# Kernel tuning notes

Hardware: AMD Instinct MI355X
Metric: run time of the kernel (lower is better)

## Reference

```python
import jax, jax.numpy as jnp
import numpy as np


def setup_inputs() -> dict:
    key = jax.random.key(0)
    kq, kk, kv = jax.random.split(key, 3)
    B, H, S, D = 2, 8, 4096, 64
    return {
        "query": jax.random.normal(kq, (B, H, S, D), dtype=jnp.float32),
        "key": jax.random.normal(kk, (B, H, S, D), dtype=jnp.float32),
        "value": jax.random.normal(kv, (B, H, S, D), dtype=jnp.float32),
    }


def reference(query, key, value):
    # NOTE: the torch source overwrites sqrt(d) with d, so the divisor is D, not sqrt(D).
    d = query.shape[-1]
    # score: [B, H, S_q, S_k]
    score = jnp.einsum("bhqd,bhkd->bhqk", query, key) / d
    relu = jax.nn.relu(score)  # no softmax / row normalization
    out = jnp.einsum("bhqk,bhkd->bhqd", relu, value)
    return out
```

## Files before the change

kernel.cpp:

```cpp
#include <hip/hip_runtime.h>
#include <hip/hip_bf16.h>
#include <stdint.h>


#define NH 16
#define SEQ 4096
#define DD 64
#define HE (SEQ*DD)
#define HB (HE*2)
#define Q16_OFF 0
#define K16_OFF (NH*HB)
#define V16_OFF (2*NH*HB)
#define WS_NEED (3*NH*HB)

typedef __attribute__((ext_vector_type(8)))  short    bf16x8;
typedef __attribute__((ext_vector_type(16))) float    f32x16;
typedef __attribute__((ext_vector_type(4)))  uint32_t u32x4;

__device__ inline uint32_t f2bf1(float f) {
  return (uint32_t)__builtin_bit_cast(unsigned short, __float2bfloat16(f));
}
__device__ inline uint32_t pack2bf(float a, float b) {
  return f2bf1(a) | (f2bf1(b) << 16);
}
__device__ inline uint32_t cvtpk(float lo, float hi) {
  uint32_t r;
  asm("v_cvt_pk_bf16_f32 %0, %1, %2" : "=v"(r) : "v"(lo), "v"(hi));
  return r;
}
__device__ inline uint32_t relu2(uint32_t w) {
  uint32_t r;
  asm("v_pk_max_f16 %0, %1, 0" : "=v"(r) : "v"(w));
  return r;
}

__global__ __launch_bounds__(256) void prepass_kernel(const float* __restrict__ Q,
                                                      const float* __restrict__ K,
                                                      const float* __restrict__ V,
                                                      char* __restrict__ ws) {
  __shared__ float vt[64*65];
  int bx = blockIdx.x, tid = threadIdx.x;
  if (bx < 2048) {
    int head = bx >> 7, qg = bx & 127;
    int r31 = tid & 31, c = tid >> 5;
    const float4* s = (const float4*)(Q + (size_t)head*HE + ((size_t)(qg*32 + r31))*64 + c*8);
    float4 a = s[0], b = s[1];
    const float sc = 1.0f/64.0f;
    u32x4 o;
    o.x = pack2bf(a.x*sc, a.y*sc);
    o.y = pack2bf(a.z*sc, a.w*sc);
    o.z = pack2bf(b.x*sc, b.y*sc);
    o.w = pack2bf(b.z*sc, b.w*sc);
    char* tb = ws + Q16_OFF + (size_t)head*HB;
    *(u32x4*)(tb + ((qg*4 + (c >> 1))*1024) + ((c & 1)*32 + r31)*16) = o;
  } else if (bx < 3072) {
    int tile = bx - 2048;
    int head = tile >> 6, t = tile & 63;
    int r = tid >> 2, c0 = (tid & 3) * 16;
    const float4* s4 = (const float4*)(K + (size_t)head*HE + ((size_t)(t*64 + r))*64 + c0);
    float4 f0 = s4[0], f1 = s4[1], f2 = s4[2], f3 = s4[3];
    u32x4 c_lo, c_hi;
    c_lo.x = pack2bf(f0.x, f0.y); c_lo.y = pack2bf(f0.z, f0.w);
    c_lo.z = pack2bf(f1.x, f1.y); c_lo.w = pack2bf(f1.z, f1.w);
    c_hi.x = pack2bf(f2.x, f2.y); c_hi.y = pack2bf(f2.z, f2.w);
    c_hi.z = pack2bf(f3.x, f3.y); c_hi.w = pack2bf(f3.z, f3.w);
    char* tb = ws + K16_OFF + ((size_t)head*64 + t)*8192;
    char* chunk = tb + ((r >> 5)*4 + (tid & 3))*1024 + (r & 31)*16;
    *(u32x4*)(chunk)       = c_lo;
    *(u32x4*)(chunk + 512) = c_hi;
  } else {
    int tile = bx - 3072;
    int head = tile >> 6, t = tile & 63;
    int k = tid >> 2, c0 = (tid & 3)*16;
    const float4* s4 = (const float4*)(V + (size_t)head*HE + ((size_t)(t*64 + k))*64 + c0);
    float4 f0 = s4[0], f1 = s4[1], f2 = s4[2], f3 = s4[3];
    float tmp[16] = {f0.x,f0.y,f0.z,f0.w, f1.x,f1.y,f1.z,f1.w,
                     f2.x,f2.y,f2.z,f2.w, f3.x,f3.y,f3.z,f3.w};
    #pragma unroll
    for (int j = 0; j < 16; ++j) vt[k*65 + c0 + j] = tmp[j];
    __syncthreads();
    int d = tid >> 2, k0 = (tid & 3)*16;
    float v2[16];
    #pragma unroll
    for (int j = 0; j < 16; ++j) v2[j] = vt[(k0 + j)*65 + d];
    u32x4 c_lo, c_hi;
    c_lo.x = pack2bf(v2[0],  v2[1]);  c_lo.y = pack2bf(v2[2],  v2[3]);
    c_lo.z = pack2bf(v2[4],  v2[5]);  c_lo.w = pack2bf(v2[6],  v2[7]);
    c_hi.x = pack2bf(v2[8],  v2[9]);  c_hi.y = pack2bf(v2[10], v2[11]);
    c_hi.z = pack2bf(v2[12], v2[13]); c_hi.w = pack2bf(v2[14], v2[15]);
    char* tb = ws + V16_OFF + ((size_t)head*64 + t)*8192;
    char* chunk = tb + ((d >> 5)*4 + (tid & 3))*1024 + (d & 31)*16;
    *(u32x4*)(chunk)       = c_lo;
    *(u32x4*)(chunk + 512) = c_hi;
  }
}

__global__ __launch_bounds__(256, 2) void attn_kernel(const char* __restrict__ ws,
                                                      float* __restrict__ out) {
  __shared__ float red[128*64];
  int bid = blockIdx.x;
  int bx = (bid & 7) * 64 + (bid >> 3);
  int head = bx >> 5, qblk = bx & 31;
  int tid = threadIdx.x;
  int lane = tid & 63, w = tid >> 6;
  int l31 = lane & 31, h = lane >> 5;
  int g  = w >> 1;
  int wg = w & 1;

  const char* q16   = ws + Q16_OFF + (size_t)head*HB;
  const char* kbase = ws + K16_OFF + (size_t)head*HB + (size_t)g*32*8192;
  const char* vbase = ws + V16_OFF + (size_t)head*HB + (size_t)g*32*8192;

  int qg0 = qblk*4 + wg*2;
  bf16x8 qf[2][4];
  #pragma unroll
  for (int m = 0; m < 2; ++m)
    #pragma unroll
    for (int t = 0; t < 4; ++t)
      qf[m][t] = *(const bf16x8*)(q16 + ((size_t)((qg0 + m)*4 + t))*1024 + lane*16);

  f32x16 kZero;
  #pragma unroll
  for (int i = 0; i < 16; ++i) kZero[i] = 0.f;

  f32x16 o[2][2];
  #pragma unroll
  for (int m = 0; m < 2; ++m)
    #pragma unroll
    for (int nd = 0; nd < 2; ++nd)
      #pragma unroll
      for (int i = 0; i < 16; ++i) o[m][nd][i] = 0.f;

  bf16x8 kfA[2][4], kfB[2][4], vf[2][4];

  auto loadK = [&](bf16x8 (&kf)[2][4], int kt) {
    const char* kp = kbase + (size_t)kt*8192;
    #pragma unroll
    for (int i = 0; i < 8; ++i)
      kf[i >> 2][i & 3] = *(const bf16x8*)(kp + i*1024 + lane*16);
  };
  auto loadV = [&](int kt) {
    const char* vp = vbase + (size_t)kt*8192;
    #pragma unroll
    for (int i = 0; i < 8; ++i)
      vf[i >> 2][i & 3] = *(const bf16x8*)(vp + i*1024 + lane*16);
  };

  auto computeT = [&](bf16x8 (&kf)[2][4]) {
    f32x16 st[2][2];
    #pragma unroll
    for (int n = 0; n < 2; ++n) {
      __builtin_amdgcn_s_setprio(1);
      #pragma unroll
      for (int m = 0; m < 2; ++m) {
        f32x16 acc = __builtin_amdgcn_mfma_f32_32x32x16_bf16(kf[n][0], qf[m][0], kZero, 0, 0, 0);
        #pragma unroll
        for (int t = 1; t < 4; ++t)
          acc = __builtin_amdgcn_mfma_f32_32x32x16_bf16(kf[n][t], qf[m][t], acc, 0, 0, 0);
        st[m][n] = acc;
      }
      __builtin_amdgcn_s_setprio(0);
    }
    bf16x8 pa[2][4];
    #pragma unroll
    for (int m = 0; m < 2; ++m)
      #pragma unroll
      for (int n = 0; n < 2; ++n)
        #pragma unroll
        for (int kn = 0; kn < 2; ++kn) {
          uint32_t w0 = cvtpk(st[m][n][kn*8+0], st[m][n][kn*8+1]);
          uint32_t w1 = cvtpk(st[m][n][kn*8+2], st[m][n][kn*8+3]);
          uint32_t w2 = cvtpk(st[m][n][kn*8+4], st[m][n][kn*8+5]);
          uint32_t w3 = cvtpk(st[m][n][kn*8+6], st[m][n][kn*8+7]);
          asm("v_permlane32_swap_b32 %0, %1" : "+v"(w0), "+v"(w2));
          asm("v_permlane32_swap_b32 %0, %1" : "+v"(w1), "+v"(w3));
          union { uint32_t u[4]; bf16x8 v; } pk;
          pk.u[0] = relu2(w0);
          pk.u[1] = relu2(w1);
          pk.u[2] = relu2(w2);
          pk.u[3] = relu2(w3);
          pa[m][n*2 + kn] = pk.v;
        }
    __builtin_amdgcn_s_setprio(1);
    #pragma unroll
    for (int m = 0; m < 2; ++m)
      #pragma unroll
      for (int nd = 0; nd < 2; ++nd)
        #pragma unroll
        for (int ks = 0; ks < 4; ++ks)
          o[m][nd] = __builtin_amdgcn_mfma_f32_32x32x16_bf16(pa[m][ks], vf[nd][ks], o[m][nd], 0, 0, 0);
    __builtin_amdgcn_s_setprio(0);
  };

  loadK(kfA, 0);
  #pragma unroll 1
  for (int kt = 0; kt < 32; kt += 2) {
    loadV(kt);
    loadK(kfB, (kt + 1) & 31);
    computeT(kfA);
    loadV(kt + 1);
    loadK(kfA, (kt + 2) & 31);
    computeT(kfB);
    if ((kt & 3) == 2) __builtin_amdgcn_s_barrier();
  }

  __syncthreads();
  if (g == 1) {
    #pragma unroll
    for (int m = 0; m < 2; ++m)
      #pragma unroll
      for (int nd = 0; nd < 2; ++nd)
        #pragma unroll
        for (int r = 0; r < 16; ++r) {
          int ql = wg*64 + m*32 + (r & 3) + 8*(r >> 2) + 4*h;
          red[ql*64 + nd*32 + l31] = o[m][nd][r];
        }
  }
  __syncthreads();
  if (g == 0) {
    float* outh = out + (size_t)head*HE;
    #pragma unroll
    for (int m = 0; m < 2; ++m)
      #pragma unroll
      for (int nd = 0; nd < 2; ++nd)
        #pragma unroll
        for (int r = 0; r < 16; ++r) {
          int ql = wg*64 + m*32 + (r & 3) + 8*(r >> 2) + 4*h;
          float v = o[m][nd][r] + red[ql*64 + nd*32 + l31];
          outh[(size_t)(qblk*128 + ql)*64 + nd*32 + l31] = v;
        }
  }
}

extern "C" void kernel_launch(void* const* d_in, const int* in_sizes, int n_in,
                              void* d_out, int out_size, void* d_ws, size_t ws_size,
                              hipStream_t stream) {
  if (n_in < 3 || ws_size < (size_t)WS_NEED) return;
  const float* Q = (const float*)d_in[0];
  const float* K = (const float*)d_in[1];
  const float* V = (const float*)d_in[2];
  float* out = (float*)d_out;
  char* ws = (char*)d_ws;
  hipLaunchKernelGGL(prepass_kernel, dim3(4096), dim3(256), 0, stream, Q, K, V, ws);
  hipLaunchKernelGGL(attn_kernel,    dim3(512),  dim3(256), 0, stream, ws, out);
}
```

Measured before the change: 92.88 us.

## Give each wave its own 32-row query tile over all keys, dropping split-K reduction

Before, the four waves formed two key-halves times two query pairs, so each wave held two 32-row query tiles and the halves were summed through shared memory. Now each wave owns one 32-row query tile and walks all 64 key tiles, writing results directly with no shared-memory reduction and fewer accumulator registers. The cost is that each K/V fragment loaded from global/L2 now feeds only one query tile instead of two, so per-wave memory traffic per MFMA doubles. The loop is also twice as long, with fewer barriers.

Result: faster. 89.84 us (-3.3%).

```diff
diff --git a/kernel.cpp b/kernel.cpp
--- a/kernel.cpp
+++ b/kernel.cpp
@@ -97,39 +97,32 @@
 
 __global__ __launch_bounds__(256, 2) void attn_kernel(const char* __restrict__ ws,
                                                       float* __restrict__ out) {
-  __shared__ float red[128*64];
   int bid = blockIdx.x;
   int bx = (bid & 7) * 64 + (bid >> 3);
   int head = bx >> 5, qblk = bx & 31;
   int tid = threadIdx.x;
   int lane = tid & 63, w = tid >> 6;
   int l31 = lane & 31, h = lane >> 5;
-  int g  = w >> 1;
-  int wg = w & 1;
 
   const char* q16   = ws + Q16_OFF + (size_t)head*HB;
-  const char* kbase = ws + K16_OFF + (size_t)head*HB + (size_t)g*32*8192;
-  const char* vbase = ws + V16_OFF + (size_t)head*HB + (size_t)g*32*8192;
-
-  int qg0 = qblk*4 + wg*2;
-  bf16x8 qf[2][4];
-  #pragma unroll
-  for (int m = 0; m < 2; ++m)
-    #pragma unroll
-    for (int t = 0; t < 4; ++t)
-      qf[m][t] = *(const bf16x8*)(q16 + ((size_t)((qg0 + m)*4 + t))*1024 + lane*16);
+  const char* kbase = ws + K16_OFF + (size_t)head*HB;
+  const char* vbase = ws + V16_OFF + (size_t)head*HB;
+
+  int qg = qblk*4 + w;
+  bf16x8 qf[4];
+  #pragma unroll
+  for (int t = 0; t < 4; ++t)
+    qf[t] = *(const bf16x8*)(q16 + ((size_t)(qg*4 + t))*1024 + lane*16);
 
   f32x16 kZero;
   #pragma unroll
   for (int i = 0; i < 16; ++i) kZero[i] = 0.f;
 
-  f32x16 o[2][2];
-  #pragma unroll
-  for (int m = 0; m < 2; ++m)
-    #pragma unroll
-    for (int nd = 0; nd < 2; ++nd)
-      #pragma unroll
-      for (int i = 0; i < 16; ++i) o[m][nd][i] = 0.f;
+  f32x16 o[2];
+  #pragma unroll
+  for (int nd = 0; nd < 2; ++nd)
+    #pragma unroll
+    for (int i = 0; i < 16; ++i) o[nd][i] = 0.f;
 
   bf16x8 kfA[2][4], kfB[2][4], vf[2][4];
 
@@ -147,89 +140,64 @@
   };
 
   auto computeT = [&](bf16x8 (&kf)[2][4]) {
-    f32x16 st[2][2];
+    f32x16 st[2];
     #pragma unroll
     for (int n = 0; n < 2; ++n) {
       __builtin_amdgcn_s_setprio(1);
+      f32x16 acc = __builtin_amdgcn_mfma_f32_32x32x16_bf16(kf[n][0], qf[0], kZero, 0, 0, 0);
       #pragma unroll
-      for (int m = 0; m < 2; ++m) {
-        f32x16 acc = __builtin_amdgcn_mfma_f32_32x32x16_bf16(kf[n][0], qf[m][0], kZero, 0, 0, 0);
-        #pragma unroll
-        for (int t = 1; t < 4; ++t)
-          acc = __builtin_amdgcn_mfma_f32_32x32x16_bf16(kf[n][t], qf[m][t], acc, 0, 0, 0);
-        st[m][n] = acc;
-      }
+      for (int t = 1; t < 4; ++t)
+        acc = __builtin_amdgcn_mfma_f32_32x32x16_bf16(kf[n][t], qf[t], acc, 0, 0, 0);
+      st[n] = acc;
       __builtin_amdgcn_s_setprio(0);
     }
-    bf16x8 pa[2][4];
-    #pragma unroll
-    for (int m = 0; m < 2; ++m)
+    bf16x8 pa[4];
+    #pragma unroll
+    for (int n = 0; n < 2; ++n)
       #pragma unroll
-      for (int n = 0; n < 2; ++n)
-        #pragma unroll
-        for (int kn = 0; kn < 2; ++kn) {
-          uint32_t w0 = cvtpk(st[m][n][kn*8+0], st[m][n][kn*8+1]);
-          uint32_t w1 = cvtpk(st[m][n][kn*8+2], st[m][n][kn*8+3]);
-          uint32_t w2 = cvtpk(st[m][n][kn*8+4], st[m][n][kn*8+5]);
-          uint32_t w3 = cvtpk(st[m][n][kn*8+6], st[m][n][kn*8+7]);
-          asm("v_permlane32_swap_b32 %0, %1" : "+v"(w0), "+v"(w2));
-          asm("v_permlane32_swap_b32 %0, %1" : "+v"(w1), "+v"(w3));
-          union { uint32_t u[4]; bf16x8 v; } pk;
-          pk.u[0] = relu2(w0);
-          pk.u[1] = relu2(w1);
-          pk.u[2] = relu2(w2);
-          pk.u[3] = relu2(w3);
-          pa[m][n*2 + kn] = pk.v;
-        }
+      for (int kn = 0; kn < 2; ++kn) {
+        uint32_t w0 = cvtpk(st[n][kn*8+0], st[n][kn*8+1]);
+        uint32_t w1 = cvtpk(st[n][kn*8+2], st[n][kn*8+3]);
+        uint32_t w2 = cvtpk(st[n][kn*8+4], st[n][kn*8+5]);
+        uint32_t w3 = cvtpk(st[n][kn*8+6], st[n][kn*8+7]);
+        asm("v_permlane32_swap_b32 %0, %1" : "+v"(w0), "+v"(w2));
+        asm("v_permlane32_swap_b32 %0, %1" : "+v"(w1), "+v"(w3));
+        union { uint32_t u[4]; bf16x8 v; } pk;
+        pk.u[0] = relu2(w0);
+        pk.u[1] = relu2(w1);
+        pk.u[2] = relu2(w2);
+        pk.u[3] = relu2(w3);
+        pa[n*2 + kn] = pk.v;
+      }
     __builtin_amdgcn_s_setprio(1);
     #pragma unroll
-    for (int m = 0; m < 2; ++m)
+    for (int nd = 0; nd < 2; ++nd)
       #pragma unroll
-      for (int nd = 0; nd < 2; ++nd)
-        #pragma unroll
-        for (int ks = 0; ks < 4; ++ks)
-          o[m][nd] = __builtin_amdgcn_mfma_f32_32x32x16_bf16(pa[m][ks], vf[nd][ks], o[m][nd], 0, 0, 0);
+      for (int ks = 0; ks < 4; ++ks)
+        o[nd] = __builtin_amdgcn_mfma_f32_32x32x16_bf16(pa[ks], vf[nd][ks], o[nd], 0, 0, 0);
     __builtin_amdgcn_s_setprio(0);
   };
 
   loadK(kfA, 0);
   #pragma unroll 1
-  for (int kt = 0; kt < 32; kt += 2) {
+  for (int kt = 0; kt < 64; kt += 2) {
     loadV(kt);
-    loadK(kfB, (kt + 1) & 31);
+    loadK(kfB, (kt + 1) & 63);
     computeT(kfA);
     loadV(kt + 1);
-    loadK(kfA, (kt + 2) & 31);
+    loadK(kfA, (kt + 2) & 63);
     computeT(kfB);
-    if ((kt & 3) == 2) __builtin_amdgcn_s_barrier();
+    if ((kt & 7) == 6) __builtin_amdgcn_s_barrier();
   }
 
-  __syncthreads();
-  if (g == 1) {
-    #pragma unroll
-    for (int m = 0; m < 2; ++m)
-      #pragma unroll
-      for (int nd = 0; nd < 2; ++nd)
-        #pragma unroll
-        for (int r = 0; r < 16; ++r) {
-          int ql = wg*64 + m*32 + (r & 3) + 8*(r >> 2) + 4*h;
-          red[ql*64 + nd*32 + l31] = o[m][nd][r];
-        }
-  }
-  __syncthreads();
-  if (g == 0) {
-    float* outh = out + (size_t)head*HE;
-    #pragma unroll
-    for (int m = 0; m < 2; ++m)
-      #pragma unroll
-      for (int nd = 0; nd < 2; ++nd)
-        #pragma unroll
-        for (int r = 0; r < 16; ++r) {
-          int ql = wg*64 + m*32 + (r & 3) + 8*(r >> 2) + 4*h;
-          float v = o[m][nd][r] + red[ql*64 + nd*32 + l31];
-          outh[(size_t)(qblk*128 + ql)*64 + nd*32 + l31] = v;
-        }
-  }
+  float* outh = out + (size_t)head*HE;
+  #pragma unroll
+  for (int nd = 0; nd < 2; ++nd)
+    #pragma unroll
+    for (int r = 0; r < 16; ++r) {
+      int ql = w*32 + (r & 3) + 8*(r >> 2) + 4*h;
+      outh[(size_t)(qblk*128 + ql)*64 + nd*32 + l31] = o[nd][r];
+    }
 }
 
 extern "C" void kernel_launch(void* const* d_in, const int* in_sizes, int n_in,
```
